# Kernel tuning notes

Measured on AMD Instinct MI355X. Metric: run time of the kernel, lower is better.

Reference implementation:

```python
import jax, jax.numpy as jnp
import numpy as np

NUM_CATS = 8
ACTION_DIM = 64
HIDDEN = 1024  # out_type.size == config.hidden_size
N_TOKENS = 4096  # B*T
N_BATCH = 128    # timesteps batch; tiled to N_TOKENS in forward


def sinusoidal_pos_encoding(t, dim):
    # standard transformer sinusoidal encoding; t: (N,) -> (N, dim)
    half = dim // 2
    div = jnp.exp(jnp.arange(half, dtype=jnp.float32) * (-np.log(10000.0) / half))
    ang = t.astype(jnp.float32)[:, None] * div[None, :]          # (N, half)
    pe = jnp.stack([jnp.sin(ang), jnp.cos(ang)], axis=-1)        # (N, half, 2)
    return pe.reshape(t.shape[0], dim)


def cat_linear(x, W, b, cat_ids):
    """Per-category linear (gather -> per-group GEMM -> scatter-back, fused).
    x: (N, din), W: (C, din, dout), b: (C, dout), cat_ids: (N,) int.
    Mathematically identical to the torch loop over unique cat ids."""
    y_all = jnp.einsum('nd,cdo->nco', x, W)                      # dense dispatch over C
    y = jnp.take_along_axis(y_all, cat_ids[:, None, None], axis=1)[:, 0, :]
    return y + b[cat_ids]


def setup_inputs() -> dict:
    key = jax.random.key(0)
    ks = jax.random.split(key, 9)
    inp = {
        'actions': jax.random.normal(ks[0], (N_TOKENS, ACTION_DIM), dtype=jnp.float32),
        'timesteps': jax.random.randint(ks[1], (N_BATCH,), 0, 1000, dtype=jnp.int32),
        'cat_ids': jax.random.randint(ks[2], (N_TOKENS,), 0, NUM_CATS, dtype=jnp.int32),
        'W1': jax.random.normal(ks[3], (NUM_CATS, ACTION_DIM, HIDDEN), dtype=jnp.float32) / np.sqrt(ACTION_DIM),
        'b1': jax.random.normal(ks[4], (NUM_CATS, HIDDEN), dtype=jnp.float32) * 0.02,
        'W2': jax.random.normal(ks[5], (NUM_CATS, 2 * HIDDEN, HIDDEN), dtype=jnp.float32) / np.sqrt(2 * HIDDEN),
        'b2': jax.random.normal(ks[6], (NUM_CATS, HIDDEN), dtype=jnp.float32) * 0.02,
        'W3': jax.random.normal(ks[7], (NUM_CATS, HIDDEN, HIDDEN), dtype=jnp.float32) / np.sqrt(HIDDEN),
        'b3': jax.random.normal(ks[8], (NUM_CATS, HIDDEN), dtype=jnp.float32) * 0.02,
    }
    return inp


def reference(actions, timesteps, cat_ids, W1, b1, W2, b2, W3, b3):
    n = actions.shape[0]
    # timesteps.repeat(B // timesteps.shape[0]) in torch tiles the whole tensor
    t_full = jnp.tile(timesteps, n // timesteps.shape[0])        # (N,)
    a_emb = cat_linear(actions, W1, b1, cat_ids)                 # (N, H)
    tau_emb = sinusoidal_pos_encoding(t_full, HIDDEN).astype(a_emb.dtype)
    x = jnp.concatenate([a_emb, tau_emb], axis=-1)               # (N, 2H)
    x = jax.nn.silu(cat_linear(x, W2, b2, cat_ids))              # swish
    x = cat_linear(x, W3, b3, cat_ids)                           # (N, H)
    return x
```

## Files before the change

kernel.cpp:

```cpp
#include <hip/hip_runtime.h>
#include <cmath>


#define NTOK 4096
#define HID  1024
#define NC   8
#define MPAD 4224

typedef _Float16 f16;
typedef _Float16 f16x8 __attribute__((ext_vector_type(8)));
typedef float    f32x4 __attribute__((ext_vector_type(4)));

#define GLDS16(g, l) __builtin_amdgcn_global_load_lds(                      \
    (const __attribute__((address_space(1))) void*)(g),                     \
    (__attribute__((address_space(3))) void*)(l), 16, 0, 0)
#define WAITV(n) asm volatile("s_waitcnt vmcnt(" #n ")" ::: "memory")

__device__ __forceinline__ int slot16(int r, int q) {
  return (r >> 1) * 8 + ((((r & 1) << 2) | q) ^ ((r >> 1) & 7));
}

__global__ void build_perm_kernel(const int* __restrict__ cat,
                                  int* __restrict__ perm,
                                  int* __restrict__ cat_off,
                                  int* __restrict__ tmap) {
  __shared__ int cnt[NC];
  __shared__ int off[NC + 1];
  const int tid = threadIdx.x;
  if (tid < NC) cnt[tid] = 0;
  __syncthreads();
  for (int n = tid; n < NTOK; n += blockDim.x) atomicAdd(&cnt[cat[n]], 1);
  __syncthreads();
  if (tid == 0) {
    int s = 0;
    for (int c = 0; c < NC; ++c) { off[c] = s; s += cnt[c]; }
    off[NC] = s;
    int ns = 0;
    for (int c = 0; c < NC; ++c) {
      const int n = off[c + 1] - off[c];
      for (int m0 = 0; m0 < n; m0 += 64) tmap[1 + ns++] = (c << 20) | m0;
    }
    tmap[0] = ns;
  }
  __syncthreads();
  if (tid < NC) cnt[tid] = off[tid];
  if (tid <= NC) cat_off[tid] = off[tid];
  __syncthreads();
  for (int n = tid; n < NTOK; n += blockDim.x) {
    int pos = atomicAdd(&cnt[cat[n]], 1);
    perm[pos] = n;
  }
}

__global__ void tau16_kernel(const int* __restrict__ ts, f16* __restrict__ tau) {
  const int b = blockIdx.x;
  const float t = (float)ts[b];
  const float cdiv = -0.017988946039015984f;
  for (int i = threadIdx.x; i < HID / 2; i += blockDim.x) {
    float ang = t * expf(cdiv * (float)i);
    tau[(size_t)b * HID + 2 * i]     = (f16)sinf(ang);
    tau[(size_t)b * HID + 2 * i + 1] = (f16)cosf(ang);
  }
}

__global__ void gather_kernel(const float* __restrict__ actions,
                              const f16* __restrict__ tau,
                              const int* __restrict__ perm,
                              f16* __restrict__ act_g, f16* __restrict__ xcat) {
  const int r = blockIdx.x;
  const int tok = perm[r];
  const int t = threadIdx.x;
  if (t < 64) act_g[(size_t)r * 64 + t] = (f16)actions[(size_t)tok * 64 + t];
  const uint4* src = (const uint4*)(tau + (size_t)(tok & 127) * HID);
  uint4* dst = (uint4*)(xcat + (size_t)r * 2048 + HID);
  dst[t] = src[t];
}

__global__ __launch_bounds__(256) void wcvt_kernel(const float* __restrict__ W,
                                                   f16* __restrict__ Wt, int K) {
  const int c = blockIdx.z, k0 = blockIdx.y * 64, n0 = blockIdx.x * 64;
  __shared__ f16 tl[64][68];
  const int tid = threadIdx.x;
  const int rr = tid >> 4, cs = (tid & 15) * 4;
  const float* src = W + ((size_t)c * K + k0) * HID + n0;
#pragma unroll
  for (int it = 0; it < 4; ++it) {
    const int kr = rr + it * 16;
    float4 v = *(const float4*)(src + (size_t)kr * HID + cs);
    tl[kr][cs + 0] = (f16)v.x;
    tl[kr][cs + 1] = (f16)v.y;
    tl[kr][cs + 2] = (f16)v.z;
    tl[kr][cs + 3] = (f16)v.w;
  }
  __syncthreads();
  f16* dst = Wt + ((size_t)c * HID + n0) * K + k0;
#pragma unroll
  for (int it = 0; it < 4; ++it) {
    const int nr = rr + it * 16;
    union { f16 h[4]; uint2 u; } pk;
    pk.h[0] = tl[cs + 0][nr];
    pk.h[1] = tl[cs + 1][nr];
    pk.h[2] = tl[cs + 2][nr];
    pk.h[3] = tl[cs + 3][nr];
    *(uint2*)(dst + (size_t)nr * K + cs) = pk.u;
  }
}

template <int K, int MODE>
__global__ __launch_bounds__(256, 4) void mfma_gemm(
    const f16* __restrict__ A, const f16* __restrict__ Wt,
    const float* __restrict__ Bias, const int* __restrict__ perm,
    const int* __restrict__ cat_off, const int* __restrict__ tmap,
    void* __restrict__ OutV) {
  constexpr int PA = (MODE == 0) ? 64 : (MODE == 1) ? 2048 : 1024;
  constexpr int BK = 32;
  constexpr int NT = K / BK;

  const int nslots = tmap[0];
  if ((int)blockIdx.y >= nslots) return;
  const int ent = tmap[1 + blockIdx.y];
  const int c = ent >> 20, m0 = ent & 0xFFF;
  const int g0 = cat_off[c], cnt = cat_off[c + 1] - g0;
  const int n0 = blockIdx.x * 64;

  __shared__ f16 As[3][64 * BK];
  __shared__ f16 Bs[3][64 * BK];
  __shared__ int rows[64];

  const int tid = threadIdx.x;
  const int lane = tid & 63, wid = tid >> 6;
  const int fr = lane & 15, fq = lane >> 4;

  if (MODE == 2 && tid < 64) {
    int m = m0 + tid;
    if (m > cnt - 1) m = cnt - 1;
    rows[tid] = perm[g0 + m];
  }

  const f16* Abase = A + (size_t)(g0 + m0) * PA;
  const f16* Bbase = Wt + ((size_t)c * HID + n0) * K;

  const int pr_ = tid >> 3, u_ = tid & 7, w_ = u_ ^ (pr_ & 7);
  const int sr_ = 2 * pr_ + (w_ >> 2), sq_ = (w_ & 3) * 8;
#define STAGE(buf, kt)                                                   \
  do {                                                                   \
    GLDS16(Abase + (size_t)sr_ * PA + (kt) + sq_, &As[buf][tid * 8]);    \
    GLDS16(Bbase + (size_t)sr_ * K + (kt) + sq_, &Bs[buf][tid * 8]);     \
  } while (0)

  f32x4 acc[4];
#pragma unroll
  for (int j = 0; j < 4; ++j) acc[j] = (f32x4){0.f, 0.f, 0.f, 0.f};

  STAGE(0, 0);
  if (NT > 1) STAGE(1, BK);

  for (int t = 0; t < NT; ++t) {
    if (t + 1 < NT) { WAITV(2); } else { WAITV(0); }
    __builtin_amdgcn_s_barrier();
    const int cur = t % 3;

    const int ar = wid * 16 + fr;
    f16x8 af = *(const f16x8*)&As[cur][slot16(ar, fq) * 8];
    f16x8 bf[4];
#pragma unroll
    for (int j = 0; j < 4; ++j) {
      const int br = j * 16 + fr;
      bf[j] = *(const f16x8*)&Bs[cur][slot16(br, fq) * 8];
    }
#pragma unroll
    for (int j = 0; j < 4; ++j)
      acc[j] = __builtin_amdgcn_mfma_f32_16x16x32_f16(af, bf[j], acc[j], 0, 0, 0);
    if (t + 2 < NT) STAGE((t + 2) % 3, (t + 2) * BK);
  }
#undef STAGE

  const int mlb = wid * 16 + fq * 4;
#pragma unroll
  for (int j = 0; j < 4; ++j) {
    const int col = j * 16 + fr;
    const float bb = Bias[c * HID + n0 + col];
#pragma unroll
    for (int q = 0; q < 4; ++q) {
      const int ml = mlb + q;
      if (m0 + ml >= cnt) continue;
      float v = acc[j][q] + bb;
      if (MODE == 1) v = v / (1.0f + __expf(-v));
      if (MODE == 2) {
        ((float*)OutV)[(size_t)rows[ml] * HID + n0 + col] = v;
      } else if (MODE == 1) {
        ((f16*)OutV)[(size_t)(g0 + m0 + ml) * HID + n0 + col] = (f16)v;
      } else {
        ((f16*)OutV)[(size_t)(g0 + m0 + ml) * 2048 + n0 + col] = (f16)v;
      }
    }
  }
}

extern "C" void kernel_launch(void* const* d_in, const int* in_sizes, int n_in,
                              void* d_out, int out_size, void* d_ws, size_t ws_size,
                              hipStream_t stream) {
  const float* actions   = (const float*)d_in[0];
  const int*   timesteps = (const int*)d_in[1];
  const int*   cat_ids   = (const int*)d_in[2];
  const float* W1 = (const float*)d_in[3];
  const float* b1 = (const float*)d_in[4];
  const float* W2 = (const float*)d_in[5];
  const float* b2 = (const float*)d_in[6];
  const float* W3 = (const float*)d_in[7];
  const float* b3 = (const float*)d_in[8];
  float* out = (float*)d_out;

  char* ws = (char*)d_ws;
  const size_t MiB = 1u << 20;
  int* perm    = (int*)(ws + 0);
  int* cat_off = (int*)(ws + (16u << 10));
  int* tmap    = (int*)(ws + (20u << 10));
  f16* tau16   = (f16*)(ws + (32u << 10));
  f16* act_g   = (f16*)(ws + (512u << 10));
  f16* Wt1     = (f16*)(ws + 2 * MiB);
  f16* xcat    = (f16*)(ws + 3 * MiB);
  f16* h       = (f16*)(ws + 20 * MiB);
  f16* Wt2     = (f16*)(ws + 29 * MiB);
  f16* Wt3     = (f16*)(ws + 61 * MiB);

  build_perm_kernel<<<1, 1024, 0, stream>>>(cat_ids, perm, cat_off, tmap);
  tau16_kernel<<<128, 256, 0, stream>>>(timesteps, tau16);
  gather_kernel<<<NTOK, 128, 0, stream>>>(actions, tau16, perm, act_g, xcat);

  wcvt_kernel<<<dim3(HID / 64, 1, NC), 256, 0, stream>>>(W1, Wt1, 64);
  wcvt_kernel<<<dim3(HID / 64, 32, NC), 256, 0, stream>>>(W2, Wt2, 2048);
  wcvt_kernel<<<dim3(HID / 64, 16, NC), 256, 0, stream>>>(W3, Wt3, 1024);

  dim3 ggrid(HID / 64, 72, 1);
  mfma_gemm<64, 0><<<ggrid, 256, 0, stream>>>(act_g, Wt1, b1, perm, cat_off, tmap, xcat);
  mfma_gemm<2048, 1><<<ggrid, 256, 0, stream>>>(xcat, Wt2, b2, perm, cat_off, tmap, h);
  mfma_gemm<1024, 2><<<ggrid, 256, 0, stream>>>(h, Wt3, b3, perm, cat_off, tmap, out);
}
```

Before: 258.1 us.

## Fold W1 into W2 and precompute tau contribution per timestep

Layers one and two are merged algebraically. W12 = W1·W2[:H] is precomputed per category, b1·W2[:H] is folded into an effective bias, and the tau half of the second GEMM is computed once for the 128 distinct timesteps per category rather than for all 4096 tokens. The main second-layer GEMM therefore shrinks from K=2048 to K=64. The GEMM pipeline also moves from 3 to 4 LDS stages. Composing the weights in fp16 may change rounding, and several small setup kernels are added.

```diff
diff --git a/kernel.cpp b/kernel.cpp
--- a/kernel.cpp
+++ b/kernel.cpp
@@ -64,16 +64,20 @@
 }
 
 __global__ void gather_kernel(const float* __restrict__ actions,
-                              const f16* __restrict__ tau,
                               const int* __restrict__ perm,
-                              f16* __restrict__ act_g, f16* __restrict__ xcat) {
+                              f16* __restrict__ act_g) {
   const int r = blockIdx.x;
   const int tok = perm[r];
-  const int t = threadIdx.x;
-  if (t < 64) act_g[(size_t)r * 64 + t] = (f16)actions[(size_t)tok * 64 + t];
-  const uint4* src = (const uint4*)(tau + (size_t)(tok & 127) * HID);
-  uint4* dst = (uint4*)(xcat + (size_t)r * 2048 + HID);
-  dst[t] = src[t];
+  act_g[(size_t)r * 64 + threadIdx.x] =
+      (f16)actions[(size_t)tok * 64 + threadIdx.x];
+}
+
+__global__ void w1cvt_kernel(const float* __restrict__ W1, f16* __restrict__ o) {
+  const int i = blockIdx.x * 256 + threadIdx.x;
+  float4 v = *(const float4*)(W1 + (size_t)i * 4);
+  union { f16 h[4]; uint2 u; } pk;
+  pk.h[0] = (f16)v.x; pk.h[1] = (f16)v.y; pk.h[2] = (f16)v.z; pk.h[3] = (f16)v.w;
+  *(uint2*)(o + (size_t)i * 4) = pk.u;
 }
 
 __global__ __launch_bounds__(256) void wcvt_kernel(const float* __restrict__ W,
@@ -106,46 +110,86 @@
   }
 }
 
-template <int K, int MODE>
+__global__ __launch_bounds__(256) void bias2eff_kernel(
+    const float* __restrict__ b1, const float* __restrict__ b2,
+    const f16* __restrict__ Wt2, float* __restrict__ out) {
+  const int c = blockIdx.y;
+  const int o = blockIdx.x * 4 + (threadIdx.x >> 6);
+  const int lane = threadIdx.x & 63;
+  const float* bp = b1 + c * HID + lane * 16;
+  const f16* wp = Wt2 + ((size_t)c * HID + o) * 2048 + lane * 16;
+  float s = 0.f;
+#pragma unroll
+  for (int u = 0; u < 4; ++u) {
+    float4 bv = *(const float4*)(bp + u * 4);
+    f16 w0 = wp[u * 4 + 0], w1 = wp[u * 4 + 1], w2 = wp[u * 4 + 2], w3 = wp[u * 4 + 3];
+    s += bv.x * (float)w0 + bv.y * (float)w1 + bv.z * (float)w2 + bv.w * (float)w3;
+  }
+#pragma unroll
+  for (int off = 32; off >= 1; off >>= 1) s += __shfl_down(s, off);
+  if (lane == 0) out[c * HID + o] = s + b2[c * HID + o];
+}
+
+template <int K, int PA, int PB, int MODE>
 __global__ __launch_bounds__(256, 4) void mfma_gemm(
-    const f16* __restrict__ A, const f16* __restrict__ Wt,
-    const float* __restrict__ Bias, const int* __restrict__ perm,
-    const int* __restrict__ cat_off, const int* __restrict__ tmap,
-    void* __restrict__ OutV) {
-  constexpr int PA = (MODE == 0) ? 64 : (MODE == 1) ? 2048 : 1024;
+    const f16* __restrict__ A, const f16* __restrict__ B,
+    const float* __restrict__ Bias, const float* __restrict__ Ttau,
+    const int* __restrict__ perm, const int* __restrict__ cat_off,
+    const int* __restrict__ tmap, void* __restrict__ OutV) {
   constexpr int BK = 32;
   constexpr int NT = K / BK;
 
-  const int nslots = tmap[0];
-  if ((int)blockIdx.y >= nslots) return;
-  const int ent = tmap[1 + blockIdx.y];
-  const int c = ent >> 20, m0 = ent & 0xFFF;
-  const int g0 = cat_off[c], cnt = cat_off[c + 1] - g0;
-  const int n0 = blockIdx.x * 64;
-
-  __shared__ f16 As[3][64 * BK];
-  __shared__ f16 Bs[3][64 * BK];
+  int c, m0, g0 = 0, cnt, n0;
+  if constexpr (MODE == 0) {
+    c = blockIdx.y >> 4; m0 = (blockIdx.y & 15) * 64; cnt = 1024; n0 = 0;
+  } else if constexpr (MODE == 1) {
+    c = blockIdx.y >> 1; m0 = (blockIdx.y & 1) * 64; cnt = 128;
+    n0 = blockIdx.x * 64;
+  } else {
+    const int nslots = tmap[0];
+    if ((int)blockIdx.y >= nslots) return;
+    const int ent = tmap[1 + blockIdx.y];
+    c = ent >> 20; m0 = ent & 0xFFF;
+    g0 = cat_off[c]; cnt = cat_off[c + 1] - g0;
+    n0 = blockIdx.x * 64;
+  }
+
+  __shared__ f16 As[4][64 * BK];
+  __shared__ f16 Bs[4][64 * BK];
   __shared__ int rows[64];
 
   const int tid = threadIdx.x;
   const int lane = tid & 63, wid = tid >> 6;
   const int fr = lane & 15, fq = lane >> 4;
 
-  if (MODE == 2 && tid < 64) {
+  if (MODE >= 2 && tid < 64) {
     int m = m0 + tid;
     if (m > cnt - 1) m = cnt - 1;
     rows[tid] = perm[g0 + m];
   }
 
-  const f16* Abase = A + (size_t)(g0 + m0) * PA;
-  const f16* Bbase = Wt + ((size_t)c * HID + n0) * K;
+  const f16* Abase;
+  const f16* Bbase;
+  if constexpr (MODE == 0) {
+    Abase = A + ((size_t)c * 1024 + m0) * 2048;
+    Bbase = B + (size_t)c * 65536;
+  } else if constexpr (MODE == 1) {
+    Abase = A + (size_t)m0 * 1024;
+    Bbase = B + ((size_t)c * 1024 + n0) * 2048 + 1024;
+  } else if constexpr (MODE == 2) {
+    Abase = A + (size_t)(g0 + m0) * 64;
+    Bbase = B + (size_t)c * 65536 + (size_t)n0 * 64;
+  } else {
+    Abase = A + (size_t)(g0 + m0) * 1024;
+    Bbase = B + ((size_t)c * 1024 + n0) * 1024;
+  }
 
   const int pr_ = tid >> 3, u_ = tid & 7, w_ = u_ ^ (pr_ & 7);
   const int sr_ = 2 * pr_ + (w_ >> 2), sq_ = (w_ & 3) * 8;
 #define STAGE(buf, kt)                                                   \
   do {                                                                   \
     GLDS16(Abase + (size_t)sr_ * PA + (kt) + sq_, &As[buf][tid * 8]);    \
-    GLDS16(Bbase + (size_t)sr_ * K + (kt) + sq_, &Bs[buf][tid * 8]);     \
+    GLDS16(Bbase + (size_t)sr_ * PB + (kt) + sq_, &Bs[buf][tid * 8]);    \
   } while (0)
 
   f32x4 acc[4];
@@ -154,24 +198,25 @@
 
   STAGE(0, 0);
   if (NT > 1) STAGE(1, BK);
+  if (NT > 2) STAGE(2, 2 * BK);
 
   for (int t = 0; t < NT; ++t) {
-    if (t + 1 < NT) { WAITV(2); } else { WAITV(0); }
+    if (t + 2 < NT) { WAITV(4); }
+    else if (t + 1 < NT) { WAITV(2); }
+    else { WAITV(0); }
     __builtin_amdgcn_s_barrier();
-    const int cur = t % 3;
+    const int cur = t & 3;
 
     const int ar = wid * 16 + fr;
     f16x8 af = *(const f16x8*)&As[cur][slot16(ar, fq) * 8];
     f16x8 bf[4];
 #pragma unroll
-    for (int j = 0; j < 4; ++j) {
-      const int br = j * 16 + fr;
-      bf[j] = *(const f16x8*)&Bs[cur][slot16(br, fq) * 8];
-    }
+    for (int j = 0; j < 4; ++j)
+      bf[j] = *(const f16x8*)&Bs[cur][slot16(j * 16 + fr, fq) * 8];
 #pragma unroll
     for (int j = 0; j < 4; ++j)
       acc[j] = __builtin_amdgcn_mfma_f32_16x16x32_f16(af, bf[j], acc[j], 0, 0, 0);
-    if (t + 2 < NT) STAGE((t + 2) % 3, (t + 2) * BK);
+    if (t + 3 < NT) STAGE((t + 3) & 3, (t + 3) * BK);
   }
 #undef STAGE
 
@@ -179,19 +224,25 @@
 #pragma unroll
   for (int j = 0; j < 4; ++j) {
     const int col = j * 16 + fr;
-    const float bb = Bias[c * HID + n0 + col];
 #pragma unroll
     for (int q = 0; q < 4; ++q) {
       const int ml = mlb + q;
-      if (m0 + ml >= cnt) continue;
-      float v = acc[j][q] + bb;
-      if (MODE == 1) v = v / (1.0f + __expf(-v));
-      if (MODE == 2) {
-        ((float*)OutV)[(size_t)rows[ml] * HID + n0 + col] = v;
-      } else if (MODE == 1) {
-        ((f16*)OutV)[(size_t)(g0 + m0 + ml) * HID + n0 + col] = (f16)v;
+      const int m = m0 + ml;
+      if constexpr (MODE == 0) {
+        ((f16*)OutV)[(size_t)c * 65536 + (size_t)m * 64 + col] = (f16)acc[j][q];
+      } else if constexpr (MODE == 1) {
+        float v = acc[j][q] + Bias[c * HID + n0 + col];
+        ((float*)OutV)[(size_t)c * 131072 + (size_t)m * 1024 + n0 + col] = v;
+      } else if constexpr (MODE == 2) {
+        if (m >= cnt) continue;
+        const int b = rows[ml] & 127;
+        float v = acc[j][q] + Ttau[((size_t)c * 128 + b) * 1024 + n0 + col];
+        v = v / (1.0f + __expf(-v));
+        ((f16*)OutV)[(size_t)(g0 + m) * 1024 + n0 + col] = (f16)v;
       } else {
-        ((f16*)OutV)[(size_t)(g0 + m0 + ml) * 2048 + n0 + col] = (f16)v;
+        if (m >= cnt) continue;
+        float v = acc[j][q] + Bias[c * HID + n0 + col];
+        ((float*)OutV)[(size_t)rows[ml] * 1024 + n0 + col] = v;
       }
     }
   }
@@ -213,27 +264,33 @@
 
   char* ws = (char*)d_ws;
   const size_t MiB = 1u << 20;
-  int* perm    = (int*)(ws + 0);
-  int* cat_off = (int*)(ws + (16u << 10));
-  int* tmap    = (int*)(ws + (20u << 10));
-  f16* tau16   = (f16*)(ws + (32u << 10));
-  f16* act_g   = (f16*)(ws + (512u << 10));
-  f16* Wt1     = (f16*)(ws + 2 * MiB);
-  f16* xcat    = (f16*)(ws + 3 * MiB);
-  f16* h       = (f16*)(ws + 20 * MiB);
-  f16* Wt2     = (f16*)(ws + 29 * MiB);
-  f16* Wt3     = (f16*)(ws + 61 * MiB);
+  int*   perm    = (int*)(ws + 0);
+  int*   cat_off = (int*)(ws + (16u << 10));
+  int*   tmap    = (int*)(ws + (20u << 10));
+  f16*   tau16   = (f16*)(ws + (32u << 10));
+  f16*   act_g   = (f16*)(ws + (512u << 10));
+  f16*   w1f16   = (f16*)(ws + 2 * MiB);
+  f16*   W12t    = (f16*)(ws + 3 * MiB);
+  float* b2eff   = (float*)(ws + 4 * MiB);
+  float* ttau    = (float*)(ws + 5 * MiB);
+  f16*   h       = (f16*)(ws + 9 * MiB);
+  f16*   Wt2     = (f16*)(ws + 18 * MiB);
+  f16*   Wt3     = (f16*)(ws + 50 * MiB);
 
   build_perm_kernel<<<1, 1024, 0, stream>>>(cat_ids, perm, cat_off, tmap);
   tau16_kernel<<<128, 256, 0, stream>>>(timesteps, tau16);
-  gather_kernel<<<NTOK, 128, 0, stream>>>(actions, tau16, perm, act_g, xcat);
-
-  wcvt_kernel<<<dim3(HID / 64, 1, NC), 256, 0, stream>>>(W1, Wt1, 64);
+  gather_kernel<<<NTOK, 64, 0, stream>>>(actions, perm, act_g);
+  w1cvt_kernel<<<512, 256, 0, stream>>>(W1, w1f16);
   wcvt_kernel<<<dim3(HID / 64, 32, NC), 256, 0, stream>>>(W2, Wt2, 2048);
   wcvt_kernel<<<dim3(HID / 64, 16, NC), 256, 0, stream>>>(W3, Wt3, 1024);
-
-  dim3 ggrid(HID / 64, 72, 1);
-  mfma_gemm<64, 0><<<ggrid, 256, 0, stream>>>(act_g, Wt1, b1, perm, cat_off, tmap, xcat);
-  mfma_gemm<2048, 1><<<ggrid, 256, 0, stream>>>(xcat, Wt2, b2, perm, cat_off, tmap, h);
-  mfma_gemm<1024, 2><<<ggrid, 256, 0, stream>>>(h, Wt3, b3, perm, cat_off, tmap, out);
-}
+  bias2eff_kernel<<<dim3(256, NC), 256, 0, stream>>>(b1, b2, Wt2, b2eff);
+
+  mfma_gemm<1024, 2048, 1024, 0><<<dim3(1, 128), 256, 0, stream>>>(
+      Wt2, w1f16, nullptr, nullptr, nullptr, nullptr, nullptr, W12t);
+  mfma_gemm<1024, 1024, 2048, 1><<<dim3(16, 16), 256, 0, stream>>>(
+      tau16, Wt2, b2eff, nullptr, nullptr, nullptr, nullptr, ttau);
+  mfma_gemm<64, 64, 64, 2><<<dim3(16, 72), 256, 0, stream>>>(
+      act_g, W12t, nullptr, ttau, perm, cat_off, tmap, h);
+  mfma_gemm<1024, 1024, 1024, 3><<<dim3(16, 72), 256, 0, stream>>>(
+      h, Wt3, b3, nullptr, perm, cat_off, tmap, out);
+}
```

Result: faster. 245.0 us (-5.1%).
